# Performance work log

Measured on AMD Instinct MI355X. Metric: run time of the kernel, lower is better.

## Reference

```python
import jax, jax.numpy as jnp
import numpy as np

D_MODEL = 2048
N_HEAD = 16
HEAD_DIM = D_MODEL // N_HEAD
SCALE = 1.0 / (HEAD_DIM ** 0.5)


def setup_inputs() -> dict:
    key = jax.random.key(0)
    kx, kq, kk, kv, ko = jax.random.split(key, 5)
    std = 1.0 / np.sqrt(D_MODEL)
    return {
        "x": jax.random.normal(kx, (2, 2048, D_MODEL), dtype=jnp.float32),
        "w_q": jax.random.normal(kq, (D_MODEL, D_MODEL), dtype=jnp.float32) * std,
        "w_k": jax.random.normal(kk, (D_MODEL, D_MODEL), dtype=jnp.float32) * std,
        "w_v": jax.random.normal(kv, (D_MODEL, D_MODEL), dtype=jnp.float32) * std,
        "w_o": jax.random.normal(ko, (D_MODEL, D_MODEL), dtype=jnp.float32) * std,
    }


def reference(x, w_q, w_k, w_v, w_o):
    b, s, d = x.shape
    # nn.Linear(d,d,bias=False): y = x @ W^T, weights stored [out, in]
    def proj(w):
        y = jnp.einsum("bsd,ed->bse", x, w)
        return y.reshape(b, s, N_HEAD, HEAD_DIM).transpose(0, 2, 1, 3)  # [b,h,s,hd]
    q, k, v = proj(w_q), proj(w_k), proj(w_v)
    scores = jnp.einsum("bhqd,bhkd->bhqk", q, k) * SCALE  # [b,h,s,s]
    probs = jax.nn.softmax(scores, axis=-1)
    attn = jnp.einsum("bhqk,bhkd->bhqd", probs, v)
    attn = attn.transpose(0, 2, 1, 3).reshape(b, s, d)
    return jnp.einsum("bsd,ed->bse", attn, w_o)
```

## Files before the change

### kernel.cpp

```cpp
#include <hip/hip_runtime.h>

#define D_MODEL 2048
#define SEQ 2048
#define BATCH 2
#define NH 16
#define HD 128
#define MTOT 4096
#define NQKV 6144
#define QSTRIDE 4096

static constexpr float SCALE_LOG2E = 0.08838834764831845f * 1.4426950408889634f;

typedef __bf16 bf16x8 __attribute__((ext_vector_type(8)));
typedef _Float16 f16x4 __attribute__((ext_vector_type(4)));
typedef float f32x4 __attribute__((ext_vector_type(4)));

__device__ inline unsigned short f2bf(float f) {
  unsigned int u = __builtin_bit_cast(unsigned int, f);
  u += 0x7fffu + ((u >> 16) & 1u);
  return (unsigned short)(u >> 16);
}

__device__ inline float fast_exp2(float x) {
#if __has_builtin(__builtin_amdgcn_exp2f)
  return __builtin_amdgcn_exp2f(x);
#else
  return exp2f(x);
#endif
}

__device__ inline void gload_lds16(const void* g, void* s) {
  __builtin_amdgcn_global_load_lds(
      (__attribute__((address_space(1))) void*)g,
      (__attribute__((address_space(3))) void*)s, 16, 0, 0);
}

#define BARX() __builtin_amdgcn_s_barrier()
#define PRIO(x) __builtin_amdgcn_s_setprio(x)
#define LGK0()                                              \
  do {                                                      \
    asm volatile("s_waitcnt lgkmcnt(0)" ::: "memory");      \
    __builtin_amdgcn_sched_barrier(0);                      \
  } while (0)
#define VMW(n) asm volatile("s_waitcnt vmcnt(" #n ")" ::: "memory")

__global__ __launch_bounds__(256) void cvt_all(
    const float* __restrict__ x, const float* __restrict__ wq,
    const float* __restrict__ wk, const float* __restrict__ wv,
    const float* __restrict__ wo, unsigned short* __restrict__ xb,
    unsigned short* __restrict__ wqkv, unsigned short* __restrict__ wob) {
  const int y = blockIdx.y;
  const float* src;
  unsigned short* dst;
  int n4;
  if (y == 0) { src = x; dst = xb; n4 = MTOT * D_MODEL / 4; }
  else if (y == 4) { src = wo; dst = wob; n4 = D_MODEL * D_MODEL / 4; }
  else {
    src = (y == 1) ? wq : (y == 2) ? wk : wv;
    dst = wqkv + (size_t)(y - 1) * D_MODEL * D_MODEL;
    n4 = D_MODEL * D_MODEL / 4;
  }
  int i = blockIdx.x * 256 + threadIdx.x;
  if (i < n4) {
    float4 v = ((const float4*)src)[i];
    ushort4 o;
    o.x = f2bf(v.x); o.y = f2bf(v.y); o.z = f2bf(v.z); o.w = f2bf(v.w);
    ((ushort4*)dst)[i] = o;
  }
}

__global__ __launch_bounds__(512, 2) void gemm_qk(
    const unsigned short* __restrict__ A, const unsigned short* __restrict__ B,
    unsigned short* __restrict__ QK) {
  extern __shared__ __align__(16) char smem[];
  const int tid = threadIdx.x;
  const int lane = tid & 63;
  const int wave = tid >> 6;
  const int quad = lane >> 4;
  const int l15 = lane & 15;
  const int bid = blockIdx.x;
  const int wgid = (bid & 7) * 32 + (bid >> 3);
  const int tm = wgid >> 4, tn = wgid & 15;
  const int m0 = tm * 256, n0 = tn * 256;
  const int wm = wave >> 2;
  const int wn = wave & 3;

  const unsigned short* Ag = A + (size_t)(m0 + wave * 8 + (lane >> 3)) * 2048 +
                             (((lane & 7) ^ (lane >> 3)) * 8);
  const unsigned short* Bg = B + (size_t)(n0 + wave * 8 + (lane >> 3)) * 2048 +
                             (((lane & 7) ^ (lane >> 3)) * 8);
  char* sd = smem + wave * 1024;

  const int arow0 = (wm * 128 + l15) * 128;
  const int brow0 = (wn * 64 + l15) * 128;
  const int sk0 = (quad ^ (l15 & 7)) * 16;
  const int sk1 = ((4 + quad) ^ (l15 & 7)) * 16;

  f32x4 acc[8][4] = {};
  bf16x8 a[4][2], bl[2][2], bh[2][2];

#define QSA(u, nb, ko) \
  gload_lds16(Ag + (size_t)(u) * 64 * 2048 + (ko), sd + (nb) * 65536 + (u) * 8192)
#define QSB(u, nb, ko) \
  gload_lds16(Bg + (size_t)(u) * 64 * 2048 + (ko), sd + (nb) * 65536 + 32768 + (u) * 8192)
#define QRA(mh, cb)                                                               \
  _Pragma("unroll") for (int mi = 0; mi < 4; mi++) {                              \
    a[mi][0] = *(const bf16x8*)(smem + (cb) * 65536 + arow0 + ((mh) * 64 + mi * 16) * 128 + sk0); \
    a[mi][1] = *(const bf16x8*)(smem + (cb) * 65536 + arow0 + ((mh) * 64 + mi * 16) * 128 + sk1); \
  }
#define QRB(dst, nh, cb)                                                          \
  _Pragma("unroll") for (int ni = 0; ni < 2; ni++) {                              \
    dst[ni][0] = *(const bf16x8*)(smem + (cb) * 65536 + 32768 + brow0 + ((nh) * 32 + ni * 16) * 128 + sk0); \
    dst[ni][1] = *(const bf16x8*)(smem + (cb) * 65536 + 32768 + brow0 + ((nh) * 32 + ni * 16) * 128 + sk1); \
  }
#define QMM(mh, bsrc, nh)                                                         \
  _Pragma("unroll") for (int mi = 0; mi < 4; mi++)                                \
  _Pragma("unroll") for (int ni = 0; ni < 2; ni++) {                              \
    acc[(mh) * 4 + mi][(nh) * 2 + ni] = __builtin_amdgcn_mfma_f32_16x16x32_bf16(  \
        a[mi][0], bsrc[ni][0], acc[(mh) * 4 + mi][(nh) * 2 + ni], 0, 0, 0);       \
    acc[(mh) * 4 + mi][(nh) * 2 + ni] = __builtin_amdgcn_mfma_f32_16x16x32_bf16(  \
        a[mi][1], bsrc[ni][1], acc[(mh) * 4 + mi][(nh) * 2 + ni], 0, 0, 0);       \
  }

  QSB(0, 0, 0); QSB(1, 0, 0); QSB(2, 0, 0); QSB(3, 0, 0);
  QSA(0, 0, 0); QSA(2, 0, 0); QSA(1, 0, 0); QSA(3, 0, 0);
  VMW(0);
  BARX();

#define QKTILE(t, cb, nb)                                                         \
  {                                                                               \
    const int ko = (((t) + 1) & 31) * 64;                                         \
                                                                         \
    QRA(0, cb); QRB(bl, 0, cb);                                                   \
    QSB(0, nb, ko); QSB(1, nb, ko);                                               \
    BARX(); LGK0(); PRIO(1); QMM(0, bl, 0); PRIO(0); BARX();                      \
                                                                         \
    QRB(bh, 1, cb);                                                               \
    QSB(2, nb, ko); QSB(3, nb, ko);                                               \
    BARX(); LGK0(); PRIO(1); QMM(0, bh, 1); PRIO(0); VMW(4); BARX();              \
                                                                         \
    QRA(1, cb);                                                                   \
    QSA(0, nb, ko); QSA(2, nb, ko);                                               \
    BARX(); LGK0(); PRIO(1); QMM(1, bl, 0); PRIO(0); BARX();                      \
                                                                         \
    QSA(1, nb, ko); QSA(3, nb, ko);                                               \
    PRIO(1); QMM(1, bh, 1); PRIO(0); VMW(2); BARX();                              \
  }

  for (int t = 0; t < 32; t += 2) {
    QKTILE(t, 0, 1);
    QKTILE(t + 1, 1, 0);
  }

#pragma unroll
  for (int mi = 0; mi < 8; mi++)
#pragma unroll
    for (int ni = 0; ni < 4; ni++) {
      const int mm = m0 + wm * 128 + mi * 16 + quad * 4;
      const int nn = n0 + wn * 64 + ni * 16 + l15;
#pragma unroll
      for (int r = 0; r < 4; r++)
        QK[(size_t)(mm + r) * QSTRIDE + nn] = f2bf(acc[mi][ni][r]);
    }
#undef QSA
#undef QSB
#undef QRA
#undef QRB
#undef QMM
#undef QKTILE
}

#define VCORE_BODY(Aptr, Bptr)                                                    \
  const int tid = threadIdx.x;                                                    \
  const int lane = tid & 63;                                                      \
  const int wave = tid >> 6;                                                      \
  const int quad = lane >> 4;                                                     \
  const int l15 = lane & 15;                                                      \
  const int bid = blockIdx.x;                                                     \
  const int wgid = (bid & 7) * 32 + (bid >> 3);                                   \
  const int tm = wgid >> 3, tn = wgid & 7;                                        \
  const int m0 = tm * 128, n0 = tn * 256;                                         \
  const int wm = wave >> 1;                                             \
  const int wn = wave & 1;                                              \
  const unsigned short* Ag = (Aptr) + (size_t)(m0 + wave * 8 + (lane >> 3)) * 2048 + \
                             (((lane & 7) ^ (lane >> 3)) * 8);                    \
  const unsigned short* Bg = (Bptr) + (size_t)(n0 + wave * 8 + (lane >> 3)) * 2048 + \
                             (((lane & 7) ^ (lane >> 3)) * 8);                    \
  char* sd = smem + wave * 1024;                                                  \
  const int arow0 = (wm * 32 + l15) * 128;                                        \
  const int brow0 = (wn * 128 + l15) * 128;                                       \
  const int sk0 = (quad ^ (l15 & 7)) * 16;                                        \
  const int sk1 = ((4 + quad) ^ (l15 & 7)) * 16;                                  \
  f32x4 acc[2][8] = {};                                                           \
  bf16x8 a[2][2], bl[4][2], bh[4][2];

#define VSA(u, nb, ko) \
  gload_lds16(Ag + (size_t)(u) * 64 * 2048 + (ko), sd + (nb) * 49152 + (u) * 8192)
#define VSB(u, nb, ko) \
  gload_lds16(Bg + (size_t)(u) * 64 * 2048 + (ko), sd + (nb) * 49152 + 16384 + (u) * 8192)
#define VRA(cb)                                                                   \
  _Pragma("unroll") for (int mi = 0; mi < 2; mi++) {                              \
    a[mi][0] = *(const bf16x8*)(smem + (cb) * 49152 + arow0 + mi * 2048 + sk0);   \
    a[mi][1] = *(const bf16x8*)(smem + (cb) * 49152 + arow0 + mi * 2048 + sk1);   \
  }
#define VRB(dst, nh, cb)                                                          \
  _Pragma("unroll") for (int ni = 0; ni < 4; ni++) {                              \
    dst[ni][0] = *(const bf16x8*)(smem + (cb) * 49152 + 16384 + brow0 + ((nh) * 64 + ni * 16) * 128 + sk0); \
    dst[ni][1] = *(const bf16x8*)(smem + (cb) * 49152 + 16384 + brow0 + ((nh) * 64 + ni * 16) * 128 + sk1); \
  }
#define VMM(bsrc, nh)                                                             \
  _Pragma("unroll") for (int mi = 0; mi < 2; mi++)                                \
  _Pragma("unroll") for (int ni = 0; ni < 4; ni++) {                              \
    acc[mi][(nh) * 4 + ni] = __builtin_amdgcn_mfma_f32_16x16x32_bf16(             \
        a[mi][0], bsrc[ni][0], acc[mi][(nh) * 4 + ni], 0, 0, 0);                  \
    acc[mi][(nh) * 4 + ni] = __builtin_amdgcn_mfma_f32_16x16x32_bf16(             \
        a[mi][1], bsrc[ni][1], acc[mi][(nh) * 4 + ni], 0, 0, 0);                  \
  }
#define VSTAGE6(nb, ko)                                                           \
  VSA(0, nb, ko); VSA(1, nb, ko); VSB(0, nb, ko);                                 \
  VSB(1, nb, ko); VSB(2, nb, ko); VSB(3, nb, ko);

#define VTILE(t, cb, nb)                                                          \
  {                                                                               \
    const int ko = (((t) + 2) & 31) * 64;                                         \
                                                                         \
    VRA(cb); VRB(bl, 0, cb);                                                      \
    VSA(0, nb, ko); VSA(1, nb, ko); VSB(0, nb, ko);                               \
    BARX(); LGK0(); PRIO(1); VMM(bl, 0); PRIO(0); BARX();                         \
                                                                         \
    VRB(bh, 1, cb);                                                               \
    VSB(1, nb, ko); VSB(2, nb, ko); VSB(3, nb, ko);                               \
    BARX(); LGK0(); PRIO(1); VMM(bh, 1); PRIO(0); VMW(6); BARX();                 \
  }

#define VCORE_LOOP()                                                              \
  VSTAGE6(0, 0);                                                                  \
  VSTAGE6(1, 64);                                                                 \
  VMW(6);                                                                         \
  BARX();                                                                         \
  for (int t = 0; t < 30; t += 3) {                                               \
    VTILE(t + 0, 0, 2);                                                           \
    VTILE(t + 1, 1, 0);                                                           \
    VTILE(t + 2, 2, 1);                                                           \
  }                                                                               \
  VTILE(30, 0, 2);                                                                \
  VTILE(31, 1, 0);

__global__ __launch_bounds__(512, 2) void gemm_v(
    const unsigned short* __restrict__ A, const unsigned short* __restrict__ B,
    unsigned short* __restrict__ Vt) {
  extern __shared__ __align__(16) char smem[];
  VCORE_BODY(A, B);
  VCORE_LOOP();

  VMW(0);
  BARX();
  unsigned short* T = (unsigned short*)smem;
  const int h0 = n0 >> 7;
  const int bb = m0 >> 11;
  const int sbase = m0 & (SEQ - 1);
#pragma unroll
  for (int mi = 0; mi < 2; mi++)
#pragma unroll
    for (int q = 0; q < 8; q++) {
      const int d = q * 16 + l15;
      const int slocal = wm * 32 + mi * 16 + quad * 4;
      f16x4 hv;
#pragma unroll
      for (int r = 0; r < 4; r++) hv[r] = (_Float16)acc[mi][q][r];
      *(f16x4*)(T + wn * 17408 + d * 136 + slocal) = hv;
    }
  BARX();
  const int hd2 = tid >> 8;
  const int d = (tid >> 1) & 127;
  const int sc = (tid & 1) * 64;
  const size_t vrow = ((size_t)((bb * NH + h0 + hd2) * HD + d)) * SEQ + sbase + sc;
#pragma unroll
  for (int j = 0; j < 8; j++) {
    float4 c4 = *(const float4*)(T + hd2 * 17408 + d * 136 + sc + j * 8);
    *(float4*)(Vt + vrow + j * 8) = c4;
  }
}

__global__ __launch_bounds__(512, 2) void gemm_out(
    const unsigned short* __restrict__ A, const unsigned short* __restrict__ B,
    float* __restrict__ C) {
  extern __shared__ __align__(16) char smem[];
  VCORE_BODY(A, B);
  VCORE_LOOP();

#pragma unroll
  for (int mi = 0; mi < 2; mi++)
#pragma unroll
    for (int q = 0; q < 8; q++) {
      const int mm = m0 + wm * 32 + mi * 16 + quad * 4;
      const int nn = n0 + wn * 128 + q * 16 + l15;
#pragma unroll
      for (int r = 0; r < 4; r++)
        C[(size_t)(mm + r) * D_MODEL + nn] = acc[mi][q][r];
    }
}

__global__ __launch_bounds__(256, 2) void flash_attn(
    const unsigned short* __restrict__ QK, const unsigned short* __restrict__ Vt,
    unsigned short* __restrict__ Og) {
  __shared__ __align__(16) unsigned short Ks[2][64 * 128];
  __shared__ __align__(16) unsigned short Vs[2][128 * 64];
  const int tid = threadIdx.x;
  const int lane = tid & 63;
  const int wave = tid >> 6;
  const int quad = lane >> 4;
  const int l15 = lane & 15;
  const int id = blockIdx.x;
  const int xr = id & 7;
  const int kk = id >> 3;
  const int bh = xr * 4 + (kk >> 4);
  const int b = bh >> 4, h = bh & 15;
  const int q0 = (kk & 15) * 128;

  const size_t kbase = (size_t)(b * SEQ) * QSTRIDE + D_MODEL + h * HD;
  const size_t vbase = (size_t)bh * HD * SEQ;

  bf16x8 qf[2][4];
#pragma unroll
  for (int t = 0; t < 2; t++)
#pragma unroll
    for (int kc = 0; kc < 4; kc++)
      qf[t][kc] = *(const bf16x8*)(QK + (size_t)(b * SEQ + q0 + wave * 32 + t * 16 + l15) * QSTRIDE +
                                   h * HD + kc * 32 + quad * 8);

  const unsigned short* kg[4];
  const unsigned short* vg[4];
  int klofs[4], vlofs[4];
#pragma unroll
  for (int i = 0; i < 4; i++) {
    int krow = wave * 16 + i * 4 + quad;
    int kc_ = l15 ^ (i * 4 + quad);
    kg[i] = QK + kbase + (size_t)krow * QSTRIDE + kc_ * 8;
    klofs[i] = (wave * 16 + i * 4) * 128;
    int vrow = wave * 32 + i * 8 + (lane >> 3);
    int vc_ = (lane & 7) ^ (lane >> 3);
    vg[i] = Vt + vbase + (size_t)vrow * SEQ + vc_ * 8;
    vlofs[i] = (wave * 32 + i * 8) * 64;
  }

#pragma unroll
  for (int i = 0; i < 4; i++) gload_lds16(kg[i], &Ks[0][klofs[i]]);
#pragma unroll
  for (int i = 0; i < 4; i++) gload_lds16(vg[i], &Vs[0][vlofs[i]]);
#pragma unroll
  for (int i = 0; i < 4; i++) { kg[i] += 64 * QSTRIDE; vg[i] += 64; }
  __builtin_amdgcn_s_waitcnt(0);
  __syncthreads();

  float lsum[2] = {0.f, 0.f};
  f32x4 Oa[2][8] = {};

  for (int it = 0; it < SEQ / 64; ++it) {
    const int cur = it & 1;
    if (it < SEQ / 64 - 1) {
#pragma unroll
      for (int i = 0; i < 4; i++) gload_lds16(kg[i], &Ks[cur ^ 1][klofs[i]]);
#pragma unroll
      for (int i = 0; i < 4; i++) gload_lds16(vg[i], &Vs[cur ^ 1][vlofs[i]]);
#pragma unroll
      for (int i = 0; i < 4; i++) { kg[i] += 64 * QSTRIDE; vg[i] += 64; }
    }

    const unsigned short* kb = &Ks[cur][0];
    f32x4 sacc[2][4] = {};
#pragma unroll
    for (int js = 0; js < 4; js++)
#pragma unroll
      for (int kc = 0; kc < 4; kc++) {
        bf16x8 kf = *(const bf16x8*)(kb + (js * 16 + l15) * 128 + (((kc * 4 + quad) ^ l15) * 8));
        sacc[0][js] = __builtin_amdgcn_mfma_f32_16x16x32_bf16(kf, qf[0][kc], sacc[0][js], 0, 0, 0);
        sacc[1][js] = __builtin_amdgcn_mfma_f32_16x16x32_bf16(kf, qf[1][kc], sacc[1][js], 0, 0, 0);
      }

    f16x4 pb[2][4];
#pragma unroll
    for (int t = 0; t < 2; t++)
#pragma unroll
      for (int js = 0; js < 4; js++)
#pragma unroll
        for (int r = 0; r < 4; r++) {
          float p = fast_exp2(sacc[t][js][r] * SCALE_LOG2E);
          lsum[t] += p;
          pb[t][js][r] = (_Float16)p;
        }

    const unsigned short* vb_ = &Vs[cur][0];
#pragma unroll
    for (int jt = 0; jt < 8; jt++)
#pragma unroll
      for (int js = 0; js < 4; js++) {
        f16x4 vf = *(const f16x4*)(vb_ + (jt * 16 + l15) * 64 +
                                   (((js * 2 + (quad >> 1)) ^ (lane & 7)) * 8) + (quad & 1) * 4);
        Oa[0][jt] = __builtin_amdgcn_mfma_f32_16x16x16f16(vf, pb[0][js], Oa[0][jt], 0, 0, 0);
        Oa[1][jt] = __builtin_amdgcn_mfma_f32_16x16x16f16(vf, pb[1][js], Oa[1][jt], 0, 0, 0);
      }

    __builtin_amdgcn_s_waitcnt(0);
    __syncthreads();
  }

  float inv[2];
#pragma unroll
  for (int t = 0; t < 2; t++) {
    float s = lsum[t];
    s += __shfl_xor(s, 16);
    s += __shfl_xor(s, 32);
    inv[t] = 1.0f / s;
  }

#pragma unroll
  for (int t = 0; t < 2; t++) {
    const size_t rowbase = (size_t)(b * SEQ + q0 + wave * 32 + t * 16 + l15) * D_MODEL + h * HD;
#pragma unroll
    for (int jt = 0; jt < 8; jt++) {
      ushort4 o;
      o.x = f2bf(Oa[t][jt][0] * inv[t]);
      o.y = f2bf(Oa[t][jt][1] * inv[t]);
      o.z = f2bf(Oa[t][jt][2] * inv[t]);
      o.w = f2bf(Oa[t][jt][3] * inv[t]);
      *(ushort4*)(Og + rowbase + jt * 16 + quad * 4) = o;
    }
  }
}

extern "C" void kernel_launch(void* const* d_in, const int* in_sizes, int n_in,
                              void* d_out, int out_size, void* d_ws, size_t ws_size,
                              hipStream_t stream) {
  const float* x = (const float*)d_in[0];
  const float* wq = (const float*)d_in[1];
  const float* wk = (const float*)d_in[2];
  const float* wv = (const float*)d_in[3];
  const float* wo = (const float*)d_in[4];
  float* out = (float*)d_out;
  char* ws = (char*)d_ws;
  const size_t MB = 1u << 20;
  if (ws_size < 96 * MB) return;

  unsigned short* xb = (unsigned short*)(ws);
  unsigned short* wqkv = (unsigned short*)(ws + 16 * MB);
  unsigned short* wob = (unsigned short*)(ws + 40 * MB);
  unsigned short* QKb = (unsigned short*)(ws + 48 * MB);
  unsigned short* Vtb = (unsigned short*)(ws + 80 * MB);
  unsigned short* Ab = xb;

  static int lds_set = 0;
  if (!lds_set) {
    hipFuncSetAttribute((const void*)gemm_qk,
                        hipFuncAttributeMaxDynamicSharedMemorySize, 131072);
    hipFuncSetAttribute((const void*)gemm_v,
                        hipFuncAttributeMaxDynamicSharedMemorySize, 147456);
    hipFuncSetAttribute((const void*)gemm_out,
                        hipFuncAttributeMaxDynamicSharedMemorySize, 147456);
    lds_set = 1;
  }

  cvt_all<<<dim3(8192, 5), 256, 0, stream>>>(x, wq, wk, wv, wo, xb, wqkv, wob);

  gemm_qk<<<256, 512, 131072, stream>>>(xb, wqkv, QKb);
  gemm_v<<<256, 512, 147456, stream>>>(xb, wqkv + (size_t)4096 * 2048, Vtb);

  flash_attn<<<512, 256, 0, stream>>>(QKb, Vtb, Ab);

  gemm_out<<<256, 512, 147456, stream>>>(Ab, wob, out);
}
```

Before: 355.5 us.

## Use bf16 16x16x32 MFMA for PV with direct global V loads and bpermute

```diff
diff --git a/kernel.cpp b/kernel.cpp
--- a/kernel.cpp
+++ b/kernel.cpp
@@ -21,12 +21,20 @@
   return (unsigned short)(u >> 16);
 }
 
+__device__ inline float bf2f(unsigned int u) {
+  return __builtin_bit_cast(float, u << 16);
+}
+
 __device__ inline float fast_exp2(float x) {
 #if __has_builtin(__builtin_amdgcn_exp2f)
   return __builtin_amdgcn_exp2f(x);
 #else
   return exp2f(x);
 #endif
+}
+
+__device__ inline unsigned int bperm(int srcLane, unsigned int v) {
+  return (unsigned int)__builtin_amdgcn_ds_bpermute(srcLane << 2, (int)v);
 }
 
 __device__ inline void gload_lds16(const void* g, void* s) {
@@ -265,10 +273,12 @@
     for (int q = 0; q < 8; q++) {
       const int d = q * 16 + l15;
       const int slocal = wm * 32 + mi * 16 + quad * 4;
-      f16x4 hv;
-#pragma unroll
-      for (int r = 0; r < 4; r++) hv[r] = (_Float16)acc[mi][q][r];
-      *(f16x4*)(T + wn * 17408 + d * 136 + slocal) = hv;
+      ushort4 hv;
+      hv.x = f2bf(acc[mi][q][0]);
+      hv.y = f2bf(acc[mi][q][1]);
+      hv.z = f2bf(acc[mi][q][2]);
+      hv.w = f2bf(acc[mi][q][3]);
+      *(ushort4*)(T + wn * 17408 + d * 136 + slocal) = hv;
     }
   BARX();
   const int hd2 = tid >> 8;
@@ -305,7 +315,6 @@
     const unsigned short* __restrict__ QK, const unsigned short* __restrict__ Vt,
     unsigned short* __restrict__ Og) {
   __shared__ __align__(16) unsigned short Ks[2][64 * 128];
-  __shared__ __align__(16) unsigned short Vs[2][128 * 64];
   const int tid = threadIdx.x;
   const int lane = tid & 63;
   const int wave = tid >> 6;
@@ -330,31 +339,33 @@
                                    h * HD + kc * 32 + quad * 8);
 
   const unsigned short* kg[4];
-  const unsigned short* vg[4];
-  int klofs[4], vlofs[4];
+  int klofs[4];
 #pragma unroll
   for (int i = 0; i < 4; i++) {
     int krow = wave * 16 + i * 4 + quad;
     int kc_ = l15 ^ (i * 4 + quad);
     kg[i] = QK + kbase + (size_t)krow * QSTRIDE + kc_ * 8;
     klofs[i] = (wave * 16 + i * 4) * 128;
-    int vrow = wave * 32 + i * 8 + (lane >> 3);
-    int vc_ = (lane & 7) ^ (lane >> 3);
-    vg[i] = Vt + vbase + (size_t)vrow * SEQ + vc_ * 8;
-    vlofs[i] = (wave * 32 + i * 8) * 64;
-  }
+  }
+
+  const unsigned short* vp[8];
+#pragma unroll
+  for (int jt = 0; jt < 8; jt++)
+    vp[jt] = Vt + vbase + (size_t)(jt * 16 + l15) * SEQ + quad * 8;
 
 #pragma unroll
   for (int i = 0; i < 4; i++) gload_lds16(kg[i], &Ks[0][klofs[i]]);
 #pragma unroll
-  for (int i = 0; i < 4; i++) gload_lds16(vg[i], &Vs[0][vlofs[i]]);
-#pragma unroll
-  for (int i = 0; i < 4; i++) { kg[i] += 64 * QSTRIDE; vg[i] += 64; }
-  __builtin_amdgcn_s_waitcnt(0);
+  for (int i = 0; i < 4; i++) kg[i] += 64 * QSTRIDE;
+  VMW(0);
   __syncthreads();
 
   float lsum[2] = {0.f, 0.f};
   f32x4 Oa[2][8] = {};
+
+  const int laA = l15 + 32 * (quad & 1);
+  const int laB = laA + 16;
+  const bool hi = quad >= 2;
 
   for (int it = 0; it < SEQ / 64; ++it) {
     const int cur = it & 1;
@@ -362,13 +373,12 @@
 #pragma unroll
       for (int i = 0; i < 4; i++) gload_lds16(kg[i], &Ks[cur ^ 1][klofs[i]]);
 #pragma unroll
-      for (int i = 0; i < 4; i++) gload_lds16(vg[i], &Vs[cur ^ 1][vlofs[i]]);
-#pragma unroll
-      for (int i = 0; i < 4; i++) { kg[i] += 64 * QSTRIDE; vg[i] += 64; }
+      for (int i = 0; i < 4; i++) kg[i] += 64 * QSTRIDE;
     }
 
     const unsigned short* kb = &Ks[cur][0];
     f32x4 sacc[2][4] = {};
+    PRIO(1);
 #pragma unroll
     for (int js = 0; js < 4; js++)
 #pragma unroll
@@ -377,31 +387,57 @@
         sacc[0][js] = __builtin_amdgcn_mfma_f32_16x16x32_bf16(kf, qf[0][kc], sacc[0][js], 0, 0, 0);
         sacc[1][js] = __builtin_amdgcn_mfma_f32_16x16x32_bf16(kf, qf[1][kc], sacc[1][js], 0, 0, 0);
       }
-
-    f16x4 pb[2][4];
+    PRIO(0);
+
+    unsigned int pw[2][4][2];
 #pragma unroll
     for (int t = 0; t < 2; t++)
 #pragma unroll
-      for (int js = 0; js < 4; js++)
-#pragma unroll
-        for (int r = 0; r < 4; r++) {
-          float p = fast_exp2(sacc[t][js][r] * SCALE_LOG2E);
-          lsum[t] += p;
-          pb[t][js][r] = (_Float16)p;
-        }
-
-    const unsigned short* vb_ = &Vs[cur][0];
-#pragma unroll
-    for (int jt = 0; jt < 8; jt++)
-#pragma unroll
       for (int js = 0; js < 4; js++) {
-        f16x4 vf = *(const f16x4*)(vb_ + (jt * 16 + l15) * 64 +
-                                   (((js * 2 + (quad >> 1)) ^ (lane & 7)) * 8) + (quad & 1) * 4);
-        Oa[0][jt] = __builtin_amdgcn_mfma_f32_16x16x16f16(vf, pb[0][js], Oa[0][jt], 0, 0, 0);
-        Oa[1][jt] = __builtin_amdgcn_mfma_f32_16x16x16f16(vf, pb[1][js], Oa[1][jt], 0, 0, 0);
+        float p0 = fast_exp2(sacc[t][js][0] * SCALE_LOG2E);
+        float p1 = fast_exp2(sacc[t][js][1] * SCALE_LOG2E);
+        float p2 = fast_exp2(sacc[t][js][2] * SCALE_LOG2E);
+        float p3 = fast_exp2(sacc[t][js][3] * SCALE_LOG2E);
+        unsigned int b0 = f2bf(p0), b1 = f2bf(p1), b2 = f2bf(p2), b3 = f2bf(p3);
+        pw[t][js][0] = b0 | (b1 << 16);
+        pw[t][js][1] = b2 | (b3 << 16);
+        lsum[t] += (bf2f(b0) + bf2f(b1)) + (bf2f(b2) + bf2f(b3));
       }
 
-    __builtin_amdgcn_s_waitcnt(0);
+    bf16x8 pb8[2][2];
+#pragma unroll
+    for (int t = 0; t < 2; t++)
+#pragma unroll
+      for (int g = 0; g < 2; g++) {
+        const int j0 = 2 * g, j1 = 2 * g + 1;
+        unsigned int a0 = bperm(laA, pw[t][j0][0]), c0 = bperm(laA, pw[t][j1][0]);
+        unsigned int a1 = bperm(laA, pw[t][j0][1]), c1 = bperm(laA, pw[t][j1][1]);
+        unsigned int a2 = bperm(laB, pw[t][j0][0]), c2 = bperm(laB, pw[t][j1][0]);
+        unsigned int a3 = bperm(laB, pw[t][j0][1]), c3 = bperm(laB, pw[t][j1][1]);
+        uint4 u;
+        u.x = hi ? c0 : a0;
+        u.y = hi ? c1 : a1;
+        u.z = hi ? c2 : a2;
+        u.w = hi ? c3 : a3;
+        pb8[t][g] = __builtin_bit_cast(bf16x8, u);
+      }
+
+    const int ko = it * 64;
+    PRIO(1);
+#pragma unroll
+    for (int jt = 0; jt < 8; jt++) {
+      bf16x8 v0 = *(const bf16x8*)(vp[jt] + ko);
+      bf16x8 v1 = *(const bf16x8*)(vp[jt] + ko + 32);
+      Oa[0][jt] = __builtin_amdgcn_mfma_f32_16x16x32_bf16(v0, pb8[0][0], Oa[0][jt], 0, 0, 0);
+      Oa[1][jt] = __builtin_amdgcn_mfma_f32_16x16x32_bf16(v0, pb8[1][0], Oa[1][jt], 0, 0, 0);
+      Oa[0][jt] = __builtin_amdgcn_mfma_f32_16x16x32_bf16(v1, pb8[0][1], Oa[0][jt], 0, 0, 0);
+      Oa[1][jt] = __builtin_amdgcn_mfma_f32_16x16x32_bf16(v1, pb8[1][1], Oa[1][jt], 0, 0, 0);
+    }
+    PRIO(0);
+
+    if (it < SEQ / 64 - 1) {
+      VMW(0);
+    }
     __syncthreads();
   }
 
```

Result: slower. 423.7 us (+19.2%).
